# Kernel tuning notes

Hardware: AMD Instinct MI355X
Metric: run time of the kernel (lower is better)

## Reference

```python
import jax, jax.numpy as jnp
import numpy as np

# ---- constants (match init_kwargs) ----
H = 16            # bit depth of location codes
TP = 8            # number of parallel location dims
N = 1 << H        # location magnitude bound
N_K = 2
N_C = 2 * H * N_K + 1   # 65 candidate locations per token
T = 512           # T_train
N_TTNBR = 64
K_VOCAB = 128
S = N_TTNBR + K_VOCAB   # 192
D = 256           # dim_eu
TEMP = 0.05


def cos_similarity(c1, c2):
    """CritiGraph frexp-based cosine: sign product * (1 - bitlength(|a|^|b| + 1)/h)."""
    sg = (2 * (c1 >= 0).astype(jnp.int32) - 1) * (2 * (c2 >= 0).astype(jnp.int32) - 1)
    x = jnp.abs(c1) ^ jnp.abs(c2)
    _, e = jnp.frexp((x + 1).astype(jnp.float32))  # exponent == bit_length(x+1)
    return sg.astype(jnp.float32) * (1.0 - e.astype(jnp.float32) / H)


def setup_inputs() -> dict:
    key = jax.random.key(0)
    ks = jax.random.split(key, 8)
    loc = lambda k, shape: jax.random.randint(k, shape, 1 - N, N, dtype=jnp.int32)
    return {
        "cur_tar": jax.random.randint(ks[0], (T,), 0, K_VOCAB, dtype=jnp.int32),
        "cnc_loc": loc(ks[1], (T, N_C, TP)),
        "sta_loc": loc(ks[2], (T, TP)),
        "ttn_loc": loc(ks[3], (T, N_TTNBR, TP)),
        "voc_loc": loc(ks[4], (T, K_VOCAB, TP)),
        "sta_emb": 0.1 * jax.random.normal(ks[5], (T, D), dtype=jnp.float32),
        "ttn_emb": 0.1 * jax.random.normal(ks[6], (T, N_TTNBR, D), dtype=jnp.float32),
        "voc_emb": 0.1 * jax.random.normal(ks[7], (T, K_VOCAB, D), dtype=jnp.float32),
    }


def reference(cur_tar, cnc_loc, sta_loc, ttn_loc, voc_loc, sta_emb, ttn_emb, voc_emb):
    # positives = dynamic neighbors ++ sampled vocab
    pos_loc = jnp.concatenate([ttn_loc, voc_loc], axis=1)      # (T, S, TP) int32
    pos_emb = jnp.concatenate([ttn_emb, voc_emb], axis=1)      # (T, S, D)

    # Euclidean-space logits
    eu_val = 20.0 * TEMP * jnp.einsum('td,tsd->ts', sta_emb, pos_emb)  # (T, S)

    # CT-space similarities
    cos_sp = cos_similarity(sta_loc[:, None, :], pos_loc)      # (T, S, TP)
    cos_sum = cos_sp.sum(axis=-1)                              # (T, S)
    # candidate location swapped into each track d (ct_val_triton math)
    cos_cp = cos_similarity(cnc_loc[:, None, :, :], pos_loc[:, :, None, :])  # (T, S, N_C, TP)
    ct_val = (cos_sum[:, :, None, None] - cos_sp[:, :, None, :] + cos_cp) / TP \
             * (20.0 * TEMP)                                   # (T, S, N_C, TP)

    # KL(eu || ct) over the dynamic neighbors
    logits_ct_dyn = ct_val[:, :N_TTNBR]                        # (T, Nn, N_C, TP)
    logits_eu_dyn = eu_val[:, :N_TTNBR]                        # (T, Nn)
    p_eu = jax.nn.softmax(logits_eu_dyn, axis=1)
    lp_eu = jax.nn.log_softmax(logits_eu_dyn, axis=1)
    lp_ct = jax.nn.log_softmax(logits_ct_dyn, axis=1)
    loss_dyn_dyn = (p_eu[:, :, None, None] * (lp_eu[:, :, None, None] - lp_ct)).sum(axis=1)  # (T, N_C, TP)

    # cross-entropy over the sampled vocab
    logits_ct_sta = ct_val[:, N_TTNBR:] / TEMP                 # (T, K, N_C, TP)
    logits_flat = logits_ct_sta.reshape(T, K_VOCAB, N_C * TP)
    log_probs = jax.nn.log_softmax(logits_flat, axis=1)        # (T, K, N_C*TP)
    idx = jnp.broadcast_to(cur_tar[:, None, None].astype(jnp.int32), (T, 1, N_C * TP))
    target_lp = jnp.take_along_axis(log_probs, idx, axis=1)[:, 0, :]  # (T, N_C*TP)
    loss_dyn_sta = -target_lp.reshape(T, N_C, TP)              # (T, N_C, TP)

    return loss_dyn_dyn, loss_dyn_sta
```

## Files before the change

kernel.cpp:

```cpp
#include <hip/hip_runtime.h>


#define Tn   512
#define NC   65
#define TPd  8
#define NTn  64
#define KV   128
#define Sn   192
#define Dn   256

#define LOG2E 1.44269504088896340736f
#define LN2   0.69314718055994530942f
#define K1D (0.0625f * 0.125f * LOG2E)
#define K0D (-0.125f * LOG2E)
#define K1S (0.0625f * 2.5f * LOG2E)
#define K0S (-2.5f * LOG2E)

__device__ __forceinline__ float exp2_fast(float x) {
#if __has_builtin(__builtin_amdgcn_exp2f)
    return __builtin_amdgcn_exp2f(x);
#else
    return exp2f(x);
#endif
}

__global__ __launch_bounds__(256, 4) void critigraph_kernel(
    const int*   __restrict__ cur_tar,
    const int*   __restrict__ cnc_loc,
    const int*   __restrict__ sta_loc,
    const int*   __restrict__ ttn_loc,
    const int*   __restrict__ voc_loc,
    const float* __restrict__ sta_emb,
    const float* __restrict__ ttn_emb,
    float*       __restrict__ out)
{
    __shared__ int2  s_ab[Sn * TPd];
    __shared__ float s_csum[Sn];
    __shared__ float s_peu[NTn];
    __shared__ float s_eu[NTn];
    __shared__ int   s_cnc[NC * TPd];
    __shared__ int   s_sta[TPd];
    __shared__ float s_dotbase[TPd];
    __shared__ float s_kl;

    const int bx   = blockIdx.x;
    const int t    = bx >> 1;
    const int half = bx & 1;
    const int c0   = half ? 33 : 0;
    const int c1   = half ? NC : 33;

    const int tid  = threadIdx.x;
    const int lane = tid & 63;
    const int wv   = tid >> 6;

    if (tid < TPd) {
        int v = sta_loc[t * TPd + tid];
        s_sta[tid] = (v < 0) ? (int)(0x80000000u | (unsigned)(-v)) : v;
    }
    for (int i = tid; i < NC * TPd; i += 256) {
        int v = cnc_loc[t * NC * TPd + i];
        s_cnc[i] = (v < 0) ? (int)(0x80000000u | (unsigned)(-v)) : v;
    }
    __syncthreads();

    for (int i = tid; i < Sn * TPd; i += 256) {
        int s = i >> 3;
        int v = (s < NTn) ? ttn_loc[t * NTn * TPd + i]
                          : voc_loc[t * KV * TPd + (i - NTn * TPd)];
        int packed = (v < 0) ? (int)(0x80000000u | (unsigned)(-v)) : v;
        int   y    = packed ^ s_sta[i & 7];
        int   x    = (y & 0x7fffffff) + 1;
        float fclz = (float)__clz(x);
        float c    = fmaf(fclz, 0.0625f, -1.0f);
        c = __int_as_float(__float_as_int(c) ^ (y & 0x80000000));
        s_ab[i] = make_int2(packed, __float_as_int(c));
    }
    {
        const float4* a4 = (const float4*)(sta_emb + (size_t)t * Dn);
        float4 a = a4[lane];
        for (int s = wv; s < NTn; s += 4) {
            const float4* b4 = (const float4*)(ttn_emb + ((size_t)t * NTn + s) * Dn);
            float4 b = b4[lane];
            float d = a.x * b.x + a.y * b.y + a.z * b.z + a.w * b.w;
            #pragma unroll
            for (int m = 1; m < 64; m <<= 1) d += __shfl_xor(d, m);
            if (lane == 0) s_eu[s] = d;
        }
    }
    __syncthreads();

    if (tid < Sn) {
        float a = 0.f;
        #pragma unroll
        for (int p = 0; p < TPd; ++p) a += __int_as_float(s_ab[tid * TPd + p].y);
        s_csum[tid] = a;
    }
    __syncthreads();

    for (int i = tid; i < Sn * TPd; i += 256) {
        int s = i >> 3;
        float sc = (s < NTn) ? (0.125f * LOG2E) : (2.5f * LOG2E);
        float sp = __int_as_float(s_ab[i].y);
        s_ab[i].y = __float_as_int((s_csum[s] - sp) * sc);
    }
    if (tid < 64) {
        float e  = s_eu[tid];
        float mx = e;
        #pragma unroll
        for (int m = 1; m < 64; m <<= 1) mx = fmaxf(mx, __shfl_xor(mx, m));
        float ex = __expf(e - mx);
        float z  = ex;
        #pragma unroll
        for (int m = 1; m < 64; m <<= 1) z += __shfl_xor(z, m);
        float pe = ex / z;
        s_peu[tid] = pe;
        float kls = pe * ((e - mx) - __logf(z));
        #pragma unroll
        for (int m = 1; m < 64; m <<= 1) kls += __shfl_xor(kls, m);
        if (tid == 0) s_kl = kls;
    }
    __syncthreads();

    if (tid < 64) {
        int g = tid & 7, j = tid >> 3;
        float a = 0.f;
        #pragma unroll
        for (int k = 0; k < 8; ++k) {
            int s = j * 8 + k;
            a = fmaf(s_peu[s], __int_as_float(s_ab[s * TPd + g].y), a);
        }
        #pragma unroll
        for (int m = 8; m < 64; m <<= 1) a += __shfl_xor(a, m);
        if (tid < TPd) s_dotbase[g] = a;
    }
    __syncthreads();

    const int g   = lane >> 3;
    const int sub = lane & 7;
    const int tar = cur_tar[t];

    float rpeu[8];
    int2  rdyn[8];
    int2  rsta[16];
    #pragma unroll
    for (int k = 0; k < 8; ++k) {
        rpeu[k] = s_peu[sub + 8 * k];
        rdyn[k] = s_ab[(sub + 8 * k) * TPd + g];
    }
    #pragma unroll
    for (int k = 0; k < 16; ++k) rsta[k] = s_ab[(NTn + sub + 8 * k) * TPd + g];
    const int2  rtar = s_ab[(NTn + tar) * TPd + g];
    const float dotb = s_dotbase[g];
    const float kl   = s_kl;

    float* out_dd = out + (size_t)t * NC * TPd;
    float* out_ds = out + (size_t)Tn * NC * TPd + (size_t)t * NC * TPd;

    for (int r = c0 + wv; r < c1; r += 4) {
        const int acnc = s_cnc[r * TPd + g];

        float sum = 0.f, dotcc = 0.f;
        #pragma unroll
        for (int k = 0; k < 8; ++k) {
            int   y    = rdyn[k].x ^ acnc;
            int   x    = (y & 0x7fffffff) + 1;
            float fclz = (float)__clz(x);
            float cc   = fmaf(fclz, K1D, K0D);
            cc = __int_as_float(__float_as_int(cc) ^ (y & 0x80000000));
            sum += exp2_fast(__int_as_float(rdyn[k].y) + cc);
            dotcc = fmaf(rpeu[k], cc, dotcc);
        }

        float sum2a = 0.f, sum2b = 0.f;
        #pragma unroll
        for (int k = 0; k < 16; ++k) {
            int   y    = rsta[k].x ^ acnc;
            int   x    = (y & 0x7fffffff) + 1;
            float fclz = (float)__clz(x);
            float cc   = fmaf(fclz, K1S, K0S);
            cc = __int_as_float(__float_as_int(cc) ^ (y & 0x80000000));
            float e = exp2_fast(__int_as_float(rsta[k].y) + cc);
            if (k & 1) sum2b += e; else sum2a += e;
        }
        float sum2 = sum2a + sum2b;

        #pragma unroll
        for (int m = 1; m < 8; m <<= 1) {
            sum   += __shfl_xor(sum, m);
            dotcc += __shfl_xor(dotcc, m);
            sum2  += __shfl_xor(sum2, m);
        }

        if (sub == 0) {
            int   y    = rtar.x ^ acnc;
            int   x    = (y & 0x7fffffff) + 1;
            float fclz = (float)__clz(x);
            float cc   = fmaf(fclz, K1S, K0S);
            cc = __int_as_float(__float_as_int(cc) ^ (y & 0x80000000));
            float tgt2 = __int_as_float(rtar.y) + cc;
            out_dd[r * TPd + g] = kl + LN2 * (__log2f(sum) - (dotb + dotcc));
            out_ds[r * TPd + g] = LN2 * (__log2f(sum2) - tgt2);
        }
    }
}

extern "C" void kernel_launch(void* const* d_in, const int* in_sizes, int n_in,
                              void* d_out, int out_size, void* d_ws, size_t ws_size,
                              hipStream_t stream) {
    (void)in_sizes; (void)n_in; (void)d_ws; (void)ws_size; (void)out_size;
    const int*   cur_tar = (const int*)  d_in[0];
    const int*   cnc_loc = (const int*)  d_in[1];
    const int*   sta_loc = (const int*)  d_in[2];
    const int*   ttn_loc = (const int*)  d_in[3];
    const int*   voc_loc = (const int*)  d_in[4];
    const float* sta_emb = (const float*)d_in[5];
    const float* ttn_emb = (const float*)d_in[6];
    critigraph_kernel<<<Tn * 2, 256, 0, stream>>>(cur_tar, cnc_loc, sta_loc, ttn_loc,
                                                  voc_loc, sta_emb, ttn_emb, (float*)d_out);
}
```

Before: 155.9 us.

## Map one block per token with thread-per-output candidate loop and fused csum

Launches one block per token instead of two half-blocks. Each thread now owns two (candidate, track) outputs and loops serially over all 64 dynamic and 128 vocab positives from shared memory. This removes the per-candidate 8-lane shuffle reductions and the duplicated setup work (location packing, embedding dot products) done by both halves. The leftover 8 outputs are handled with a 32-lane reduction. The cosine sums are now reduced with shuffles during load, which removes one sync phase. It also packs p_eu into an int4 shared layout and relaxes launch_bounds to 2 blocks per SM. The tradeoff is half as many blocks and longer serial loops per thread.

```diff
diff --git a/kernel.cpp b/kernel.cpp
--- a/kernel.cpp
+++ b/kernel.cpp
@@ -8,6 +8,7 @@
 #define KV   128
 #define Sn   192
 #define Dn   256
+#define OUT1 (Tn * NC * TPd)
 
 #define LOG2E 1.44269504088896340736f
 #define LN2   0.69314718055994530942f
@@ -23,8 +24,18 @@
     return exp2f(x);
 #endif
 }
-
-__global__ __launch_bounds__(256, 4) void critigraph_kernel(
+__device__ __forceinline__ int pack_loc(int v) {
+    return (v < 0) ? (int)(0x80000000u | (unsigned)(-v)) : v;
+}
+__device__ __forceinline__ float asf(int v) { return __int_as_float(v); }
+
+__device__ __forceinline__ float cos_cc(int y, float k1, float k0) {
+    int   x  = (y & 0x7fffffff) + 1;
+    float cc = fmaf((float)__clz(x), k1, k0);
+    return __int_as_float(__float_as_int(cc) ^ (y & 0x80000000));
+}
+
+__global__ __launch_bounds__(256, 2) void critigraph_kernel(
     const int*   __restrict__ cur_tar,
     const int*   __restrict__ cnc_loc,
     const int*   __restrict__ sta_loc,
@@ -34,74 +45,71 @@
     const float* __restrict__ ttn_emb,
     float*       __restrict__ out)
 {
-    __shared__ int2  s_ab[Sn * TPd];
+    __shared__ int4  s_dyn4[NTn * TPd];
+    __shared__ int2  s_sta2[KV * TPd];
+    __shared__ int   s_cnc[NC * TPd];
+    __shared__ int   s_staloc[TPd];
     __shared__ float s_csum[Sn];
+    __shared__ float s_eu[NTn];
     __shared__ float s_peu[NTn];
-    __shared__ float s_eu[NTn];
-    __shared__ int   s_cnc[NC * TPd];
-    __shared__ int   s_sta[TPd];
     __shared__ float s_dotbase[TPd];
     __shared__ float s_kl;
 
-    const int bx   = blockIdx.x;
-    const int t    = bx >> 1;
-    const int half = bx & 1;
-    const int c0   = half ? 33 : 0;
-    const int c1   = half ? NC : 33;
-
-    const int tid  = threadIdx.x;
-    const int lane = tid & 63;
-    const int wv   = tid >> 6;
-
-    if (tid < TPd) {
-        int v = sta_loc[t * TPd + tid];
-        s_sta[tid] = (v < 0) ? (int)(0x80000000u | (unsigned)(-v)) : v;
-    }
-    for (int i = tid; i < NC * TPd; i += 256) {
-        int v = cnc_loc[t * NC * TPd + i];
-        s_cnc[i] = (v < 0) ? (int)(0x80000000u | (unsigned)(-v)) : v;
-    }
-    __syncthreads();
-
-    for (int i = tid; i < Sn * TPd; i += 256) {
+    const int t   = blockIdx.x;
+    const int tid = threadIdx.x;
+
+    if (tid < TPd) s_staloc[tid] = pack_loc(sta_loc[t * TPd + tid]);
+    for (int i = tid; i < NC * TPd; i += 256)
+        s_cnc[i] = pack_loc(cnc_loc[t * NC * TPd + i]);
+    __syncthreads();
+
+    const int mysta = s_staloc[tid & 7];
+    float mysp[6];
+    #pragma unroll
+    for (int k = 0; k < 6; ++k) {
+        int i = tid + 256 * k;
         int s = i >> 3;
         int v = (s < NTn) ? ttn_loc[t * NTn * TPd + i]
                           : voc_loc[t * KV * TPd + (i - NTn * TPd)];
-        int packed = (v < 0) ? (int)(0x80000000u | (unsigned)(-v)) : v;
-        int   y    = packed ^ s_sta[i & 7];
-        int   x    = (y & 0x7fffffff) + 1;
-        float fclz = (float)__clz(x);
-        float c    = fmaf(fclz, 0.0625f, -1.0f);
+        int packed = pack_loc(v);
+        int y = packed ^ mysta;
+        int x = (y & 0x7fffffff) + 1;
+        float c = fmaf((float)__clz(x), 0.0625f, -1.0f);
         c = __int_as_float(__float_as_int(c) ^ (y & 0x80000000));
-        s_ab[i] = make_int2(packed, __float_as_int(c));
+        mysp[k] = c;
+        if (s < NTn) s_dyn4[i].x = packed;
+        else         s_sta2[i - NTn * TPd].x = packed;
+        float v8 = c;
+        v8 += __shfl_xor(v8, 1);
+        v8 += __shfl_xor(v8, 2);
+        v8 += __shfl_xor(v8, 4);
+        if ((tid & 7) == 0) s_csum[s] = v8;
     }
     {
-        const float4* a4 = (const float4*)(sta_emb + (size_t)t * Dn);
-        float4 a = a4[lane];
-        for (int s = wv; s < NTn; s += 4) {
-            const float4* b4 = (const float4*)(ttn_emb + ((size_t)t * NTn + s) * Dn);
-            float4 b = b4[lane];
-            float d = a.x * b.x + a.y * b.y + a.z * b.z + a.w * b.w;
-            #pragma unroll
-            for (int m = 1; m < 64; m <<= 1) d += __shfl_xor(d, m);
-            if (lane == 0) s_eu[s] = d;
-        }
-    }
-    __syncthreads();
-
-    if (tid < Sn) {
-        float a = 0.f;
-        #pragma unroll
-        for (int p = 0; p < TPd; ++p) a += __int_as_float(s_ab[tid * TPd + p].y);
-        s_csum[tid] = a;
-    }
-    __syncthreads();
-
-    for (int i = tid; i < Sn * TPd; i += 256) {
+        const int r = tid >> 2, q = tid & 3;
+        const float4* A = (const float4*)(sta_emb + (size_t)t * Dn);
+        const float4* B = (const float4*)(ttn_emb + ((size_t)t * NTn + r) * Dn);
+        float acc = 0.f;
+        #pragma unroll
+        for (int k = 0; k < 16; ++k) {
+            float4 a = A[k * 4 + q];
+            float4 b = B[k * 4 + q];
+            acc += a.x * b.x + a.y * b.y + a.z * b.z + a.w * b.w;
+        }
+        acc += __shfl_xor(acc, 1);
+        acc += __shfl_xor(acc, 2);
+        if (q == 0) s_eu[r] = acc;
+    }
+    __syncthreads();
+
+    #pragma unroll
+    for (int k = 0; k < 6; ++k) {
+        int i = tid + 256 * k;
         int s = i >> 3;
         float sc = (s < NTn) ? (0.125f * LOG2E) : (2.5f * LOG2E);
-        float sp = __int_as_float(s_ab[i].y);
-        s_ab[i].y = __float_as_int((s_csum[s] - sp) * sc);
+        float b2 = (s_csum[s] - mysp[k]) * sc;
+        if (s < NTn) s_dyn4[i].y = __float_as_int(b2);
+        else         s_sta2[i - NTn * TPd].y = __float_as_int(b2);
     }
     if (tid < 64) {
         float e  = s_eu[tid];
@@ -121,13 +129,18 @@
     }
     __syncthreads();
 
+    #pragma unroll
+    for (int k = 0; k < 2; ++k) {
+        int i = tid + 256 * k;
+        s_dyn4[i].z = __float_as_int(s_peu[i >> 3]);
+    }
     if (tid < 64) {
         int g = tid & 7, j = tid >> 3;
         float a = 0.f;
         #pragma unroll
         for (int k = 0; k < 8; ++k) {
-            int s = j * 8 + k;
-            a = fmaf(s_peu[s], __int_as_float(s_ab[s * TPd + g].y), a);
+            int s = 8 * j + k;
+            a = fmaf(s_peu[s], asf(s_dyn4[s * TPd + g].y), a);
         }
         #pragma unroll
         for (int m = 8; m < 64; m <<= 1) a += __shfl_xor(a, m);
@@ -135,71 +148,80 @@
     }
     __syncthreads();
 
-    const int g   = lane >> 3;
-    const int sub = lane & 7;
-    const int tar = cur_tar[t];
-
-    float rpeu[8];
-    int2  rdyn[8];
-    int2  rsta[16];
-    #pragma unroll
-    for (int k = 0; k < 8; ++k) {
-        rpeu[k] = s_peu[sub + 8 * k];
-        rdyn[k] = s_ab[(sub + 8 * k) * TPd + g];
-    }
-    #pragma unroll
-    for (int k = 0; k < 16; ++k) rsta[k] = s_ab[(NTn + sub + 8 * k) * TPd + g];
-    const int2  rtar = s_ab[(NTn + tar) * TPd + g];
-    const float dotb = s_dotbase[g];
-    const float kl   = s_kl;
-
-    float* out_dd = out + (size_t)t * NC * TPd;
-    float* out_ds = out + (size_t)Tn * NC * TPd + (size_t)t * NC * TPd;
-
-    for (int r = c0 + wv; r < c1; r += 4) {
-        const int acnc = s_cnc[r * TPd + g];
-
-        float sum = 0.f, dotcc = 0.f;
-        #pragma unroll
-        for (int k = 0; k < 8; ++k) {
-            int   y    = rdyn[k].x ^ acnc;
-            int   x    = (y & 0x7fffffff) + 1;
-            float fclz = (float)__clz(x);
-            float cc   = fmaf(fclz, K1D, K0D);
-            cc = __int_as_float(__float_as_int(cc) ^ (y & 0x80000000));
-            sum += exp2_fast(__int_as_float(rdyn[k].y) + cc);
-            dotcc = fmaf(rpeu[k], cc, dotcc);
-        }
-
-        float sum2a = 0.f, sum2b = 0.f;
-        #pragma unroll
-        for (int k = 0; k < 16; ++k) {
-            int   y    = rsta[k].x ^ acnc;
-            int   x    = (y & 0x7fffffff) + 1;
-            float fclz = (float)__clz(x);
-            float cc   = fmaf(fclz, K1S, K0S);
-            cc = __int_as_float(__float_as_int(cc) ^ (y & 0x80000000));
-            float e = exp2_fast(__int_as_float(rsta[k].y) + cc);
-            if (k & 1) sum2b += e; else sum2a += e;
-        }
-        float sum2 = sum2a + sum2b;
-
-        #pragma unroll
-        for (int m = 1; m < 8; m <<= 1) {
-            sum   += __shfl_xor(sum, m);
-            dotcc += __shfl_xor(dotcc, m);
-            sum2  += __shfl_xor(sum2, m);
-        }
-
+    const int p     = tid & 7;
+    const int acnc1 = s_cnc[tid];
+    const int acnc2 = s_cnc[tid + 256];
+    const int tar   = cur_tar[t];
+    const float kl  = s_kl;
+    const float dtb = s_dotbase[p];
+
+    float sumA = 0.f, dotA = 0.f, sumB = 0.f, dotB = 0.f;
+    #pragma unroll 16
+    for (int s = 0; s < NTn; ++s) {
+        int4  ab = s_dyn4[s * TPd + p];
+        float bb = asf(ab.y);
+        float pe = asf(ab.z);
+        float ccA = cos_cc(ab.x ^ acnc1, K1D, K0D);
+        sumA += exp2_fast(bb + ccA);
+        dotA  = fmaf(pe, ccA, dotA);
+        float ccB = cos_cc(ab.x ^ acnc2, K1D, K0D);
+        sumB += exp2_fast(bb + ccB);
+        dotB  = fmaf(pe, ccB, dotB);
+    }
+    float s2A = 0.f, s2B = 0.f;
+    #pragma unroll 16
+    for (int v = 0; v < KV; ++v) {
+        int2  ab = s_sta2[v * TPd + p];
+        float bb = asf(ab.y);
+        s2A += exp2_fast(bb + cos_cc(ab.x ^ acnc1, K1S, K0S));
+        s2B += exp2_fast(bb + cos_cc(ab.x ^ acnc2, K1S, K0S));
+    }
+    {
+        int2  tt = s_sta2[tar * TPd + p];
+        float bt = asf(tt.y);
+        float tA = bt + cos_cc(tt.x ^ acnc1, K1S, K0S);
+        float tB = bt + cos_cc(tt.x ^ acnc2, K1S, K0S);
+        float* od = out + (size_t)t * NC * TPd;
+        float* os = out + OUT1 + (size_t)t * NC * TPd;
+        od[tid]       = kl + LN2 * (__log2f(sumA) - (dtb + dotA));
+        od[tid + 256] = kl + LN2 * (__log2f(sumB) - (dtb + dotB));
+        os[tid]       = LN2 * (__log2f(s2A) - tA);
+        os[tid + 256] = LN2 * (__log2f(s2B) - tB);
+    }
+
+    {
+        const int w    = tid >> 6;
+        const int lane = tid & 63;
+        const int half = lane >> 5;
+        const int sub  = lane & 31;
+        const int pt   = 2 * w + half;
+        const int acnct = s_cnc[512 + pt];
+        float sumd = 0.f, dotd = 0.f, sums = 0.f;
+        #pragma unroll
+        for (int k = 0; k < 2; ++k) {
+            int4 ab = s_dyn4[(sub + 32 * k) * TPd + pt];
+            float cc = cos_cc(ab.x ^ acnct, K1D, K0D);
+            sumd += exp2_fast(asf(ab.y) + cc);
+            dotd  = fmaf(asf(ab.z), cc, dotd);
+        }
+        #pragma unroll
+        for (int k = 0; k < 4; ++k) {
+            int2 ab = s_sta2[(sub + 32 * k) * TPd + pt];
+            sums += exp2_fast(asf(ab.y) + cos_cc(ab.x ^ acnct, K1S, K0S));
+        }
+        #pragma unroll
+        for (int m = 1; m < 32; m <<= 1) {
+            sumd += __shfl_xor(sumd, m);
+            dotd += __shfl_xor(dotd, m);
+            sums += __shfl_xor(sums, m);
+        }
         if (sub == 0) {
-            int   y    = rtar.x ^ acnc;
-            int   x    = (y & 0x7fffffff) + 1;
-            float fclz = (float)__clz(x);
-            float cc   = fmaf(fclz, K1S, K0S);
-            cc = __int_as_float(__float_as_int(cc) ^ (y & 0x80000000));
-            float tgt2 = __int_as_float(rtar.y) + cc;
-            out_dd[r * TPd + g] = kl + LN2 * (__log2f(sum) - (dotb + dotcc));
-            out_ds[r * TPd + g] = LN2 * (__log2f(sum2) - tgt2);
+            int2  tt = s_sta2[tar * TPd + pt];
+            float tT = asf(tt.y) + cos_cc(tt.x ^ acnct, K1S, K0S);
+            out[(size_t)t * NC * TPd + 512 + pt] =
+                kl + LN2 * (__log2f(sumd) - (s_dotbase[pt] + dotd));
+            out[OUT1 + (size_t)t * NC * TPd + 512 + pt] =
+                LN2 * (__log2f(sums) - tT);
         }
     }
 }
@@ -215,6 +237,6 @@
     const int*   voc_loc = (const int*)  d_in[4];
     const float* sta_emb = (const float*)d_in[5];
     const float* ttn_emb = (const float*)d_in[6];
-    critigraph_kernel<<<Tn * 2, 256, 0, stream>>>(cur_tar, cnc_loc, sta_loc, ttn_loc,
-                                                  voc_loc, sta_emb, ttn_emb, (float*)d_out);
-}
+    critigraph_kernel<<<Tn, 256, 0, stream>>>(cur_tar, cnc_loc, sta_loc, ttn_loc,
+                                              voc_loc, sta_emb, ttn_emb, (float*)d_out);
+}
```

New measurement: 142.8 us. -8.4%, faster.
